# Optimization experiments

Hardware: AMD Instinct MI355X
Metric: run time of the kernel (lower is better)

Reference implementation:

```python
import jax, jax.numpy as jnp
import numpy as np

N_NODES = 100000
N_EDGES = 1600000
IN_CH = 128
OUT_CH = 64


def setup_inputs() -> dict:
    key = jax.random.key(0)
    k1, k2, k3 = jax.random.split(key, 3)
    x = jax.random.normal(k1, (N_NODES, IN_CH), dtype=jnp.float32)
    edge_index = jax.random.randint(k2, (2, N_EDGES), 0, N_NODES, dtype=jnp.int64)
    # Glorot-style init for the GCN weight, zero bias (PyG defaults)
    W = jax.random.normal(k3, (IN_CH, OUT_CH), dtype=jnp.float32) * (1.0 / np.sqrt(IN_CH))
    b = jnp.zeros((OUT_CH,), dtype=jnp.float32)
    return {"x": x, "edge_index": edge_index, "W": W, "b": b}


def reference(x, edge_index, W, b):
    n = x.shape[0]
    # add self loops (GCNConv default add_self_loops=True)
    loop = jnp.arange(n, dtype=edge_index.dtype)
    row = jnp.concatenate([edge_index[0], loop])  # source
    col = jnp.concatenate([edge_index[1], loop])  # target
    # symmetric degree normalization on augmented graph
    deg = jax.ops.segment_sum(jnp.ones_like(col, dtype=x.dtype), col, num_segments=n)
    dinv = jnp.where(deg > 0, jax.lax.rsqrt(deg), 0.0)
    norm = dinv[row] * dinv[col]  # [E+N]
    # linear transform first (out_channels < in_channels), then gather-scale-scatter
    h = x @ W  # [N, OUT]
    msgs = h[row] * norm[:, None]  # [E+N, OUT]
    out = jax.ops.segment_sum(msgs, col, num_segments=n)  # [N, OUT]
    return out + b
```

## Files before the change

### kernel.cpp

```cpp
#include <hip/hip_runtime.h>
#include <hip/hip_bf16.h>


#define IN_CH 128
#define OUT_CH 64
#define BSHIFT 7
#define BNODES 128
#define MAX_NB 800
#define CH_EDGES 7168
#define SORT_CAP 4096

__device__ __forceinline__ unsigned short f2b(float f) {
    unsigned int u = __float_as_uint(f);
    return (unsigned short)((u + 0x7FFFu + ((u >> 16) & 1u)) >> 16);
}

__global__ __launch_bounds__(1024) void count_kernel(const int* __restrict__ col,
                                                     int* __restrict__ blkcnt,
                                                     int E, int NBLK, int NB) {
    __shared__ int h[MAX_NB];
    int tid = threadIdx.x;
    for (int i = tid; i < NB; i += 1024) h[i] = 0;
    __syncthreads();
    int e0 = blockIdx.x * CH_EDGES;
    #pragma unroll
    for (int r = 0; r < CH_EDGES / 1024; ++r) {
        int e = e0 + r * 1024 + tid;
        if (e < E) atomicAdd(&h[col[e] >> BSHIFT], 1);
    }
    __syncthreads();
    for (int i = tid; i < NB; i += 1024) blkcnt[i * NBLK + blockIdx.x] = h[i];
}

__global__ __launch_bounds__(256) void scan1_kernel(const int* __restrict__ v_in,
                                                    int* __restrict__ partial, int n) {
    __shared__ int s[256];
    int tid = threadIdx.x;
    int i   = blockIdx.x * 256 + tid;
    int v   = (i < n) ? v_in[i] : 0;
    s[tid] = v; __syncthreads();
    #pragma unroll
    for (int off = 1; off < 256; off <<= 1) {
        int t = (tid >= off) ? s[tid - off] : 0;
        __syncthreads();
        s[tid] += t;
        __syncthreads();
    }
    if (tid == 255) partial[blockIdx.x] = s[255];
}

__global__ __launch_bounds__(1024) void scan2_kernel(int* __restrict__ partial, int nb) {
    __shared__ int s[1024];
    int tid = threadIdx.x;
    int v   = (tid < nb) ? partial[tid] : 0;
    s[tid] = v; __syncthreads();
    #pragma unroll
    for (int off = 1; off < 1024; off <<= 1) {
        int t = (tid >= off) ? s[tid - off] : 0;
        __syncthreads();
        s[tid] += t;
        __syncthreads();
    }
    if (tid < nb) partial[tid] = s[tid] - v;
}

__global__ __launch_bounds__(256) void scan3_kernel(const int* __restrict__ v_in,
                                                    const int* __restrict__ partial,
                                                    int* __restrict__ v_out,
                                                    int* __restrict__ bucket_start,
                                                    int n, int NBLK, int NB, int E) {
    __shared__ int s[256];
    int tid = threadIdx.x;
    int i   = blockIdx.x * 256 + tid;
    int v   = (i < n) ? v_in[i] : 0;
    s[tid] = v; __syncthreads();
    #pragma unroll
    for (int off = 1; off < 256; off <<= 1) {
        int t = (tid >= off) ? s[tid - off] : 0;
        __syncthreads();
        s[tid] += t;
        __syncthreads();
    }
    if (i < n) {
        int excl = partial[blockIdx.x] + s[tid] - v;
        v_out[i] = excl;
        if (i % NBLK == 0) bucket_start[i / NBLK] = excl;
    }
    if (i == 0) bucket_start[NB] = E;
}

__global__ __launch_bounds__(1024) void place_kernel(const int* __restrict__ row,
                                                     const int* __restrict__ col,
                                                     const int* __restrict__ blkoff,
                                                     int* __restrict__ pairs,
                                                     int E, int NBLK, int NB) {
    __shared__ int cur[MAX_NB];
    int tid = threadIdx.x;
    for (int i = tid; i < NB; i += 1024) cur[i] = blkoff[i * NBLK + blockIdx.x];
    __syncthreads();
    int e0 = blockIdx.x * CH_EDGES;
    #pragma unroll
    for (int r2 = 0; r2 < CH_EDGES / 1024; ++r2) {
        int e = e0 + r2 * 1024 + tid;
        if (e < E) {
            int c = col[e];
            int b = c >> BSHIFT;
            int pos = atomicAdd(&cur[b], 1);
            pairs[pos] = row[e] | ((c & (BNODES - 1)) << 17);
        }
    }
}

__global__ __launch_bounds__(256) void bucket_sort_kernel(
    const int* __restrict__ bucket_start, const int* __restrict__ pairs,
    int* __restrict__ csr_row, int* __restrict__ row_start,
    float* __restrict__ dinv, int n, int E)
{
    __shared__ int cnt[BNODES];
    __shared__ int deg[BNODES];
    __shared__ int cur[BNODES];
    __shared__ int sorted[SORT_CAP];

    int b = blockIdx.x, tid = threadIdx.x;
    int node0 = b << BSHIFT;
    int nodeCnt = min(BNODES, n - node0);
    int s0 = bucket_start[b], s1 = bucket_start[b + 1];
    int m = s1 - s0;

    if (tid < BNODES) cnt[tid] = 0;
    __syncthreads();
    for (int e = s0 + tid; e < s1; e += 256) atomicAdd(&cnt[pairs[e] >> 17], 1);
    __syncthreads();
    if (tid < BNODES) deg[tid] = cnt[tid];
    __syncthreads();
    #pragma unroll
    for (int off = 1; off < BNODES; off <<= 1) {
        int t = (tid >= off && tid < BNODES) ? cnt[tid - off] : 0;
        __syncthreads();
        if (tid < BNODES) cnt[tid] += t;
        __syncthreads();
    }
    if (tid < BNODES) {
        int excl = cnt[tid] - deg[tid];
        cur[tid] = excl;
        if (tid < nodeCnt) {
            row_start[node0 + tid] = s0 + excl;
            dinv[node0 + tid] = rsqrtf((float)(deg[tid] + 1));
        }
    }
    if (b == gridDim.x - 1 && tid == 0) row_start[n] = E;
    __syncthreads();

    if (m <= SORT_CAP) {
        for (int e = s0 + tid; e < s1; e += 256) {
            int p   = pairs[e];
            int pos = atomicAdd(&cur[p >> 17], 1);
            sorted[pos] = p & 0x1FFFF;
        }
        __syncthreads();
        for (int i = tid; i < m; i += 256) csr_row[s0 + i] = sorted[i];
    } else {
        if (tid < BNODES) cur[tid] += s0;
        __syncthreads();
        for (int e = s0 + tid; e < s1; e += 256) {
            int p   = pairs[e];
            int pos = atomicAdd(&cur[p >> 17], 1);
            csr_row[pos] = p & 0x1FFFF;
        }
    }
}

__device__ __forceinline__ void fma4(float4& a, float s, const float4& v) {
    a.x = fmaf(s, v.x, a.x);
    a.y = fmaf(s, v.y, a.y);
    a.z = fmaf(s, v.z, a.z);
    a.w = fmaf(s, v.w, a.w);
}

__global__ __launch_bounds__(256) void gemm_kernel(
    const float* __restrict__ x, const float* __restrict__ W,
    const float* __restrict__ dinv, unsigned short* __restrict__ hpb, int n)
{
    __shared__ float xl[64 * 128];
    __shared__ float wl[128 * 64];

    int tid  = threadIdx.x;
    int row0 = blockIdx.x * 64;

    {
        const float4* wg = (const float4*)W;
        float4* wls = (float4*)wl;
        #pragma unroll
        for (int i = 0; i < 8; ++i) wls[tid + i * 256] = wg[tid + i * 256];
    }
    {
        float4* xls = (float4*)xl;
        #pragma unroll
        for (int i = 0; i < 8; ++i) {
            int f  = tid + i * 256;
            int r  = f >> 5;
            int c0 = f & 31;
            int gr = row0 + r;
            float4 v = make_float4(0.f, 0.f, 0.f, 0.f);
            if (gr < n) v = ((const float4*)(x + (size_t)gr * IN_CH))[c0];
            xls[(r << 5) | (c0 ^ (r & 7))] = v;
        }
    }
    __syncthreads();

    int tr = tid & 15;
    int tc = tid >> 4;

    float4 acc0 = {0,0,0,0}, acc1 = {0,0,0,0}, acc2 = {0,0,0,0}, acc3 = {0,0,0,0};
    const float4* xl4 = (const float4*)xl;
    const float4* wl4 = (const float4*)wl;

    #pragma unroll 4
    for (int k4 = 0; k4 < 32; ++k4) {
        int sc = k4 ^ (tr & 7);
        float4 xa0 = xl4[((tr     ) << 5) | sc];
        float4 xa1 = xl4[((tr + 16) << 5) | sc];
        float4 xa2 = xl4[((tr + 32) << 5) | sc];
        float4 xa3 = xl4[((tr + 48) << 5) | sc];
        float4 wb0 = wl4[((k4 * 4 + 0) << 4) | tc];
        float4 wb1 = wl4[((k4 * 4 + 1) << 4) | tc];
        float4 wb2 = wl4[((k4 * 4 + 2) << 4) | tc];
        float4 wb3 = wl4[((k4 * 4 + 3) << 4) | tc];

        fma4(acc0, xa0.x, wb0); fma4(acc0, xa0.y, wb1); fma4(acc0, xa0.z, wb2); fma4(acc0, xa0.w, wb3);
        fma4(acc1, xa1.x, wb0); fma4(acc1, xa1.y, wb1); fma4(acc1, xa1.z, wb2); fma4(acc1, xa1.w, wb3);
        fma4(acc2, xa2.x, wb0); fma4(acc2, xa2.y, wb1); fma4(acc2, xa2.z, wb2); fma4(acc2, xa2.w, wb3);
        fma4(acc3, xa3.x, wb0); fma4(acc3, xa3.y, wb1); fma4(acc3, xa3.z, wb2); fma4(acc3, xa3.w, wb3);
    }

    float4 accs[4] = {acc0, acc1, acc2, acc3};
    #pragma unroll
    for (int i = 0; i < 4; ++i) {
        int gr = row0 + tr + 16 * i;
        if (gr < n) {
            float di = dinv[gr];
            float4 a = accs[i];
            ushort4 h4;
            h4.x = f2b(a.x * di); h4.y = f2b(a.y * di);
            h4.z = f2b(a.z * di); h4.w = f2b(a.w * di);
            ((ushort4*)(hpb + (size_t)gr * OUT_CH))[tc] = h4;
        }
    }
}

__global__ __launch_bounds__(256) void aggregate_kernel(
    const int* __restrict__ row_start, const int* __restrict__ csr_row,
    const unsigned short* __restrict__ hpb, const float* __restrict__ dinv,
    const float* __restrict__ bias, float* __restrict__ out, int n)
{
    int wid  = (blockIdx.x * 256 + threadIdx.x) >> 6;
    int lane = threadIdx.x & 63;
    if (wid >= n) return;
    int half = lane >> 5;
    int hl   = lane & 31;

    const unsigned int* hp32 = (const unsigned int*)hpb;

    int s0 = row_start[wid];
    int s1 = row_start[wid + 1];

    float a0l=0.f,a0h=0.f,a1l=0.f,a1h=0.f,a2l=0.f,a2h=0.f,a3l=0.f,a3h=0.f;

    for (int base = s0; base < s1; base += 64) {
        int cnt  = min(64, s1 - base);
        int ridx = (base + lane < s1) ? csr_row[base + lane] : 0;
        int j = 0;
        for (; j + 8 <= cnt; j += 8) {
            int r0 = __shfl(ridx, j     + half);
            int r1 = __shfl(ridx, j + 2 + half);
            int r2 = __shfl(ridx, j + 4 + half);
            int r3 = __shfl(ridx, j + 6 + half);
            unsigned int v0 = hp32[(size_t)r0 * 32 + hl];
            unsigned int v1 = hp32[(size_t)r1 * 32 + hl];
            unsigned int v2 = hp32[(size_t)r2 * 32 + hl];
            unsigned int v3 = hp32[(size_t)r3 * 32 + hl];
            a0l += __uint_as_float(v0 << 16); a0h += __uint_as_float(v0 & 0xFFFF0000u);
            a1l += __uint_as_float(v1 << 16); a1h += __uint_as_float(v1 & 0xFFFF0000u);
            a2l += __uint_as_float(v2 << 16); a2h += __uint_as_float(v2 & 0xFFFF0000u);
            a3l += __uint_as_float(v3 << 16); a3h += __uint_as_float(v3 & 0xFFFF0000u);
        }
        for (; j < cnt; j += 2) {
            int e = j + half;
            int r = __shfl(ridx, e);
            unsigned int v = (e < cnt) ? hp32[(size_t)r * 32 + hl] : 0u;
            a0l += __uint_as_float(v << 16); a0h += __uint_as_float(v & 0xFFFF0000u);
        }
    }
    float sl = ((a0l + a1l) + (a2l + a3l));
    float sh = ((a0h + a1h) + (a2h + a3h));
    sl += __shfl_xor(sl, 32);
    sh += __shfl_xor(sh, 32);

    if (half == 0) {
        unsigned int sv = hp32[(size_t)wid * 32 + hl];
        sl += __uint_as_float(sv << 16);
        sh += __uint_as_float(sv & 0xFFFF0000u);
        float d = dinv[wid];
        float2 bb = ((const float2*)bias)[hl];
        float2 o;
        o.x = fmaf(d, sl, bb.x);
        o.y = fmaf(d, sh, bb.y);
        ((float2*)(out + (size_t)wid * OUT_CH))[hl] = o;
    }
}

extern "C" void kernel_launch(void* const* d_in, const int* in_sizes, int n_in,
                              void* d_out, int out_size, void* d_ws, size_t ws_size,
                              hipStream_t stream) {
    const float* x  = (const float*)d_in[0];
    const int*   ei = (const int*)d_in[1];
    const float* W  = (const float*)d_in[2];
    const float* b  = (const float*)d_in[3];
    float*       out = (float*)d_out;

    int n = in_sizes[0] / IN_CH;
    int E = in_sizes[1] / 2;
    const int* row = ei;
    const int* col = ei + E;

    int NB   = (n + BNODES - 1) >> BSHIFT;
    int NBLK = (E + CH_EDGES - 1) / CH_EDGES;
    int TOT  = NB * NBLK;
    int nbs  = (TOT + 255) / 256;

    char* ws = (char*)d_ws;
    int*   blkcnt       = (int*)ws;   ws += (size_t)TOT * 4;
    int*   blkoff       = (int*)ws;   ws += (size_t)TOT * 4;
    int*   partial      = (int*)ws;   ws += 1024 * 4;
    int*   bucket_start = (int*)ws;   ws += (size_t)(NB + 1) * 4;
    int*   row_start    = (int*)ws;   ws += (size_t)(n + 1) * 4;
    float* dinv         = (float*)ws; ws += (size_t)n * 4;
    int*   csr_row      = (int*)ws;   ws += (size_t)E * 4;
    ws = (char*)(((uintptr_t)ws + 255) & ~(uintptr_t)255);
    int*            pairs = (int*)ws;
    unsigned short* hpb   = (unsigned short*)ws;

    count_kernel      <<<NBLK, 1024, 0, stream>>>(col, blkcnt, E, NBLK, NB);
    scan1_kernel      <<<nbs, 256, 0, stream>>>(blkcnt, partial, TOT);
    scan2_kernel      <<<1, 1024, 0, stream>>>(partial, nbs);
    scan3_kernel      <<<nbs, 256, 0, stream>>>(blkcnt, partial, blkoff, bucket_start,
                                                TOT, NBLK, NB, E);
    place_kernel      <<<NBLK, 1024, 0, stream>>>(row, col, blkoff, pairs, E, NBLK, NB);
    bucket_sort_kernel<<<NB, 256, 0, stream>>>(bucket_start, pairs, csr_row, row_start, dinv, n, E);
    gemm_kernel       <<<(n + 63) / 64, 256, 0, stream>>>(x, W, dinv, hpb, n);
    aggregate_kernel  <<<(n + 3) / 4, 256, 0, stream>>>(row_start, csr_row, hpb, dinv, b, out, n);
}
```

Before: 208.3 us.

## Use bf16 MFMA for the feature transform GEMM with pre-transposed weights

Replaces the FP32 FMA GEMM with bf16 MFMA 16x16x32 instructions. A small prep kernel converts W to bf16 and transposes it, and x is pre-scaled by dinv and converted to bf16 while being staged into padded shared memory. Results go back through shared memory as bf16 so the global stores are coalesced. This cuts ALU and LDS time in the GEMM, at the cost of lower precision because x itself is now rounded to bf16, plus one extra small kernel launch.

```diff
diff --git a/kernel.cpp b/kernel.cpp
--- a/kernel.cpp
+++ b/kernel.cpp
@@ -9,10 +9,21 @@
 #define MAX_NB 800
 #define CH_EDGES 7168
 #define SORT_CAP 4096
+#define XSTR 136
+
+typedef short bf16x8 __attribute__((ext_vector_type(8)));
+typedef float f32x4  __attribute__((ext_vector_type(4)));
 
 __device__ __forceinline__ unsigned short f2b(float f) {
     unsigned int u = __float_as_uint(f);
     return (unsigned short)((u + 0x7FFFu + ((u >> 16) & 1u)) >> 16);
+}
+
+__global__ __launch_bounds__(256) void wprep_kernel(const float* __restrict__ W,
+                                                    unsigned short* __restrict__ wbt) {
+    int t = blockIdx.x * 256 + threadIdx.x;
+    int k = t >> 6, nn = t & 63;
+    wbt[nn * IN_CH + k] = f2b(W[t]);
 }
 
 __global__ __launch_bounds__(1024) void count_kernel(const int* __restrict__ col,
@@ -170,80 +181,88 @@
     }
 }
 
-__device__ __forceinline__ void fma4(float4& a, float s, const float4& v) {
-    a.x = fmaf(s, v.x, a.x);
-    a.y = fmaf(s, v.y, a.y);
-    a.z = fmaf(s, v.z, a.z);
-    a.w = fmaf(s, v.w, a.w);
-}
-
 __global__ __launch_bounds__(256) void gemm_kernel(
-    const float* __restrict__ x, const float* __restrict__ W,
+    const float* __restrict__ x, const unsigned short* __restrict__ wbt,
     const float* __restrict__ dinv, unsigned short* __restrict__ hpb, int n)
 {
-    __shared__ float xl[64 * 128];
-    __shared__ float wl[128 * 64];
+    __shared__ __align__(16) unsigned short xl[64 * XSTR];
+    __shared__ __align__(16) unsigned short wl[64 * XSTR];
 
     int tid  = threadIdx.x;
     int row0 = blockIdx.x * 64;
 
     {
-        const float4* wg = (const float4*)W;
-        float4* wls = (float4*)wl;
+        const uint4* src = (const uint4*)wbt;
         #pragma unroll
-        for (int i = 0; i < 8; ++i) wls[tid + i * 256] = wg[tid + i * 256];
-    }
+        for (int i = 0; i < 4; ++i) {
+            int flat = tid + i * 256;
+            int nn = flat >> 4, c = flat & 15;
+            *(uint4*)(wl + nn * XSTR + c * 8) = src[flat];
+        }
+    }
+    #pragma unroll
+    for (int i = 0; i < 4; ++i) {
+        int r  = (tid >> 4) + i * 16;
+        int c  = tid & 15;
+        int gr = row0 + r;
+        float4 v0 = make_float4(0.f,0.f,0.f,0.f), v1 = v0;
+        float d = 0.f;
+        if (gr < n) {
+            d = dinv[gr];
+            const float4* xr = (const float4*)(x + (size_t)gr * IN_CH);
+            v0 = xr[c * 2]; v1 = xr[c * 2 + 1];
+        }
+        uint4 p;
+        p.x = ((unsigned)f2b(v0.y * d) << 16) | f2b(v0.x * d);
+        p.y = ((unsigned)f2b(v0.w * d) << 16) | f2b(v0.z * d);
+        p.z = ((unsigned)f2b(v1.y * d) << 16) | f2b(v1.x * d);
+        p.w = ((unsigned)f2b(v1.w * d) << 16) | f2b(v1.z * d);
+        *(uint4*)(xl + r * XSTR + c * 8) = p;
+    }
+    __syncthreads();
+
+    int lane = tid & 63, w = tid >> 6;
+    int mrow = lane & 15;
+    int g    = lane >> 4;
+
+    f32x4 acc0 = {0,0,0,0}, acc1 = {0,0,0,0}, acc2 = {0,0,0,0}, acc3 = {0,0,0,0};
+    const unsigned short* xbase = xl + (w * 16 + mrow) * XSTR + g * 8;
+    const unsigned short* wbase = wl + mrow * XSTR + g * 8;
+
+    #pragma unroll
+    for (int k4 = 0; k4 < 4; ++k4) {
+        bf16x8 a  = *(const bf16x8*)(xbase + k4 * 32);
+        bf16x8 b0 = *(const bf16x8*)(wbase +             k4 * 32);
+        bf16x8 b1 = *(const bf16x8*)(wbase + 16 * XSTR + k4 * 32);
+        bf16x8 b2 = *(const bf16x8*)(wbase + 32 * XSTR + k4 * 32);
+        bf16x8 b3 = *(const bf16x8*)(wbase + 48 * XSTR + k4 * 32);
+        acc0 = __builtin_amdgcn_mfma_f32_16x16x32_bf16(a, b0, acc0, 0, 0, 0);
+        acc1 = __builtin_amdgcn_mfma_f32_16x16x32_bf16(a, b1, acc1, 0, 0, 0);
+        acc2 = __builtin_amdgcn_mfma_f32_16x16x32_bf16(a, b2, acc2, 0, 0, 0);
+        acc3 = __builtin_amdgcn_mfma_f32_16x16x32_bf16(a, b3, acc3, 0, 0, 0);
+    }
+    __syncthreads();
+
     {
-        float4* xls = (float4*)xl;
+        int cm = g * 4;
         #pragma unroll
-        for (int i = 0; i < 8; ++i) {
-            int f  = tid + i * 256;
-            int r  = f >> 5;
-            int c0 = f & 31;
-            int gr = row0 + r;
-            float4 v = make_float4(0.f, 0.f, 0.f, 0.f);
-            if (gr < n) v = ((const float4*)(x + (size_t)gr * IN_CH))[c0];
-            xls[(r << 5) | (c0 ^ (r & 7))] = v;
-        }
-    }
-    __syncthreads();
-
-    int tr = tid & 15;
-    int tc = tid >> 4;
-
-    float4 acc0 = {0,0,0,0}, acc1 = {0,0,0,0}, acc2 = {0,0,0,0}, acc3 = {0,0,0,0};
-    const float4* xl4 = (const float4*)xl;
-    const float4* wl4 = (const float4*)wl;
-
-    #pragma unroll 4
-    for (int k4 = 0; k4 < 32; ++k4) {
-        int sc = k4 ^ (tr & 7);
-        float4 xa0 = xl4[((tr     ) << 5) | sc];
-        float4 xa1 = xl4[((tr + 16) << 5) | sc];
-        float4 xa2 = xl4[((tr + 32) << 5) | sc];
-        float4 xa3 = xl4[((tr + 48) << 5) | sc];
-        float4 wb0 = wl4[((k4 * 4 + 0) << 4) | tc];
-        float4 wb1 = wl4[((k4 * 4 + 1) << 4) | tc];
-        float4 wb2 = wl4[((k4 * 4 + 2) << 4) | tc];
-        float4 wb3 = wl4[((k4 * 4 + 3) << 4) | tc];
-
-        fma4(acc0, xa0.x, wb0); fma4(acc0, xa0.y, wb1); fma4(acc0, xa0.z, wb2); fma4(acc0, xa0.w, wb3);
-        fma4(acc1, xa1.x, wb0); fma4(acc1, xa1.y, wb1); fma4(acc1, xa1.z, wb2); fma4(acc1, xa1.w, wb3);
-        fma4(acc2, xa2.x, wb0); fma4(acc2, xa2.y, wb1); fma4(acc2, xa2.z, wb2); fma4(acc2, xa2.w, wb3);
-        fma4(acc3, xa3.x, wb0); fma4(acc3, xa3.y, wb1); fma4(acc3, xa3.z, wb2); fma4(acc3, xa3.w, wb3);
-    }
-
-    float4 accs[4] = {acc0, acc1, acc2, acc3};
-    #pragma unroll
-    for (int i = 0; i < 4; ++i) {
-        int gr = row0 + tr + 16 * i;
+        for (int r = 0; r < 4; ++r) {
+            unsigned short* crow = xl + (w * 16 + cm + r) * XSTR + mrow;
+            crow[ 0] = f2b(acc0[r]);
+            crow[16] = f2b(acc1[r]);
+            crow[32] = f2b(acc2[r]);
+            crow[48] = f2b(acc3[r]);
+        }
+    }
+    __syncthreads();
+    #pragma unroll
+    for (int i = 0; i < 2; ++i) {
+        int flat = tid + i * 256;
+        int r = flat >> 3, c = flat & 7;
+        int gr = row0 + r;
         if (gr < n) {
-            float di = dinv[gr];
-            float4 a = accs[i];
-            ushort4 h4;
-            h4.x = f2b(a.x * di); h4.y = f2b(a.y * di);
-            h4.z = f2b(a.z * di); h4.w = f2b(a.w * di);
-            ((ushort4*)(hpb + (size_t)gr * OUT_CH))[tc] = h4;
+            uint4 v = *(const uint4*)(xl + r * XSTR + c * 8);
+            *(uint4*)(hpb + (size_t)gr * OUT_CH + c * 8) = v;
         }
     }
 }
@@ -336,10 +355,12 @@
     int*   row_start    = (int*)ws;   ws += (size_t)(n + 1) * 4;
     float* dinv         = (float*)ws; ws += (size_t)n * 4;
     int*   csr_row      = (int*)ws;   ws += (size_t)E * 4;
+    unsigned short* wbt = (unsigned short*)ws; ws += (size_t)IN_CH * OUT_CH * 2;
     ws = (char*)(((uintptr_t)ws + 255) & ~(uintptr_t)255);
     int*            pairs = (int*)ws;
     unsigned short* hpb   = (unsigned short*)ws;
 
+    wprep_kernel      <<<(IN_CH * OUT_CH) / 256, 256, 0, stream>>>(W, wbt);
     count_kernel      <<<NBLK, 1024, 0, stream>>>(col, blkcnt, E, NBLK, NB);
     scan1_kernel      <<<nbs, 256, 0, stream>>>(blkcnt, partial, TOT);
     scan2_kernel      <<<1, 1024, 0, stream>>>(partial, nbs);
@@ -347,6 +368,6 @@
                                                 TOT, NBLK, NB, E);
     place_kernel      <<<NBLK, 1024, 0, stream>>>(row, col, blkoff, pairs, E, NBLK, NB);
     bucket_sort_kernel<<<NB, 256, 0, stream>>>(bucket_start, pairs, csr_row, row_start, dinv, n, E);
-    gemm_kernel       <<<(n + 63) / 64, 256, 0, stream>>>(x, W, dinv, hpb, n);
+    gemm_kernel       <<<(n + 63) / 64, 256, 0, stream>>>(x, wbt, dinv, hpb, n);
     aggregate_kernel  <<<(n + 3) / 4, 256, 0, stream>>>(row_start, csr_row, hpb, dinv, b, out, n);
 }
```

Result: faster. 184.8 us (-11.3%).
